# Performance work log

Hardware: AMD Instinct MI355X
Metric: run time of the kernel (lower is better)

Reference implementation:

```python
import jax, jax.numpy as jnp
import numpy as np

D_MODEL = 1024
N_HEADS = 16
D_K = 64
SEQ = 4096
BATCH = 1


def setup_inputs() -> dict:
    key = jax.random.key(0)
    ks = jax.random.split(key, 6)
    s = 1.0 / np.sqrt(D_MODEL)
    return {
        "h": jax.random.normal(ks[0], (BATCH, SEQ, D_MODEL), jnp.float32),
        "gamma": jnp.ones((D_MODEL,), jnp.float32),
        "beta": jnp.zeros((D_MODEL,), jnp.float32),
        "Wq": jax.random.normal(ks[1], (D_MODEL, N_HEADS * D_K), jnp.float32) * s,
        "bq": jnp.zeros((N_HEADS * D_K,), jnp.float32),
        "Wk": jax.random.normal(ks[2], (D_MODEL, N_HEADS * D_K), jnp.float32) * s,
        "bk": jnp.zeros((N_HEADS * D_K,), jnp.float32),
        "Wv": jax.random.normal(ks[3], (D_MODEL, N_HEADS * D_K), jnp.float32) * s,
        "bv": jnp.zeros((N_HEADS * D_K,), jnp.float32),
        "Wo": jax.random.normal(ks[4], (N_HEADS * D_K, D_MODEL), jnp.float32) * s,
        "bo": jnp.zeros((D_MODEL,), jnp.float32),
    }


def _rope(x):
    # x: [b, s, h, d]
    d = x.shape[-1]
    d2 = d // 2
    theta = 1.0 / (10000.0 ** (jnp.arange(0, d, 2, dtype=jnp.float32) / d))  # [d2]
    pos = jnp.arange(x.shape[1], dtype=jnp.float32)  # [s]
    idx_theta = pos[:, None] * theta[None, :]  # [s, d2]
    idx_theta2 = jnp.concatenate([idx_theta, idx_theta], axis=-1)  # [s, d]
    cos = jnp.cos(idx_theta2)[None, :, None, :]
    sin = jnp.sin(idx_theta2)[None, :, None, :]
    neg_half = jnp.concatenate([-x[..., d2:], x[..., :d2]], axis=-1)
    return x * cos + neg_half * sin


def reference(h, gamma, beta, Wq, bq, Wk, bk, Wv, bv, Wo, bo):
    b, s, dm = h.shape
    h_res = h
    # LayerNorm (eps=1e-5, matching torch default)
    mu = jnp.mean(h, axis=-1, keepdims=True)
    var = jnp.var(h, axis=-1, keepdims=True)
    hn = (h - mu) * jax.lax.rsqrt(var + 1e-5) * gamma + beta
    mh = (b, s, N_HEADS, D_K)
    q = (hn @ Wq + bq).reshape(mh)
    k = (hn @ Wk + bk).reshape(mh)
    v = (hn @ Wv + bv).reshape(mh)
    q = _rope(q)
    k = _rope(k)
    scale = 1.0 / np.sqrt(D_K)
    attn = jnp.einsum('bihd,bjhd->bhij', q, k) * scale  # [b,h,s,s]
    # causal mask
    mask = jnp.tril(jnp.ones((s, s), dtype=bool))
    attn = jnp.where(mask, attn, -jnp.inf)
    attn = jax.nn.softmax(attn, axis=-1)
    out = jnp.einsum('bhij,bjhd->bihd', attn, v).reshape(b, s, N_HEADS * D_K)
    return out @ Wo + bo + h_res
```

## Files before the change

### kernel.cpp

```cpp
#include <hip/hip_runtime.h>
#include <stdint.h>

#define SEQLEN 4096
#define DMODEL 1024
#define NHEADS 16
#define DKDIM  64

typedef unsigned short u16;
typedef unsigned int   u32;
using f32x4 = __attribute__((ext_vector_type(4))) float;
using i32x4 = __attribute__((ext_vector_type(4))) int;
using i32x2 = __attribute__((ext_vector_type(2))) int;
using u16x8 = __attribute__((ext_vector_type(8))) unsigned short;

__device__ __forceinline__ u16 f2bf(float f) {
    u32 x = __builtin_bit_cast(u32, f);
    u32 r = x + 0x7fffu + ((x >> 16) & 1u);
    return (u16)(r >> 16);
}
__device__ __forceinline__ float exp2a(float x) {
    float r; asm("v_exp_f32 %0, %1" : "=v"(r) : "v"(x)); return r;
}
__device__ __forceinline__ u32 cvtpk(float lo, float hi) {
    u32 r; asm("v_cvt_pk_bf16_f32 %0, %1, %2" : "=v"(r) : "v"(lo), "v"(hi)); return r;
}

__device__ __forceinline__ void mfma_bf16(f32x4& d, i32x4 a, i32x4 b) {
    asm("v_mfma_f32_16x16x32_bf16 %0, %1, %2, %0" : "+v"(d) : "v"(a), "v"(b));
}
__device__ __forceinline__ void mfma16_bf16(f32x4& d, i32x2 a, i32x2 b) {
    asm("v_mfma_f32_16x16x16_bf16 %0, %1, %2, %0" : "+v"(d) : "v"(a), "v"(b));
}

#define ASYNC_COPY16(gsrc, ldst) \
    __builtin_amdgcn_global_load_lds((const __attribute__((address_space(1))) void*)(gsrc), \
                                     (__attribute__((address_space(3))) void*)(ldst), 16, 0, 0)

__global__ __launch_bounds__(256) void prep_kernel(const float* __restrict__ Wq,
                                                   const float* __restrict__ Wk,
                                                   const float* __restrict__ Wv,
                                                   const float* __restrict__ Wo,
                                                   u16* __restrict__ wqkvT,
                                                   u16* __restrict__ woT,
                                                   const float* __restrict__ h,
                                                   const float* __restrict__ gamma,
                                                   const float* __restrict__ beta,
                                                   u16* __restrict__ hn,
                                                   float* __restrict__ cosT,
                                                   float* __restrict__ sinT) {
    __shared__ float tile[32][33];
    __shared__ float red[8];
    int bid = blockIdx.x;
    int t = threadIdx.x;
    if (bid < 4096) {
        int z = bid >> 10;
        int rem = bid & 1023;
        const float* W = (z == 0) ? Wq : (z == 1) ? Wk : (z == 2) ? Wv : Wo;
        u16* Wt = (z < 3) ? wqkvT + (size_t)z * DMODEL * DMODEL : woT;
        int bx = (rem & 31) * 32;
        int by = (rem >> 5) * 32;
        int tx = t & 31, ty = t >> 5;
#pragma unroll
        for (int i = 0; i < 32; i += 8)
            tile[ty + i][tx] = W[(size_t)(by + ty + i) * DMODEL + bx + tx];
        __syncthreads();
#pragma unroll
        for (int i = 0; i < 32; i += 8)
            Wt[(size_t)(bx + ty + i) * DMODEL + by + tx] = f2bf(tile[tx][ty + i]);
    } else if (bid < 8192) {
        int row = bid - 4096;
        float4 v = reinterpret_cast<const float4*>(h + (size_t)row * DMODEL)[t];
        float s  = v.x + v.y + v.z + v.w;
        float s2 = v.x*v.x + v.y*v.y + v.z*v.z + v.w*v.w;
#pragma unroll
        for (int off = 1; off < 64; off <<= 1) {
            s  += __shfl_xor(s, off);
            s2 += __shfl_xor(s2, off);
        }
        int wid = t >> 6, lane = t & 63;
        if (lane == 0) { red[wid] = s; red[4 + wid] = s2; }
        __syncthreads();
        s  = red[0] + red[1] + red[2] + red[3];
        s2 = red[4] + red[5] + red[6] + red[7];
        float mu   = s * (1.0f / DMODEL);
        float rstd = rsqrtf(s2 * (1.0f / DMODEL) - mu * mu + 1e-5f);
        float4 g = reinterpret_cast<const float4*>(gamma)[t];
        float4 b = reinterpret_cast<const float4*>(beta)[t];
        ushort4 o;
        o.x = f2bf((v.x - mu) * rstd * g.x + b.x);
        o.y = f2bf((v.y - mu) * rstd * g.y + b.y);
        o.z = f2bf((v.z - mu) * rstd * g.z + b.z);
        o.w = f2bf((v.w - mu) * rstd * g.w + b.w);
        reinterpret_cast<ushort4*>(hn + (size_t)row * DMODEL)[t] = o;
    } else {
        int idx = (bid - 8192) * 256 + t;
        int s = idx >> 5, i = idx & 31;
        float theta = powf(10000.0f, -2.0f * (float)i / 64.0f);
        float ang = (float)s * theta;
        cosT[idx] = cosf(ang);
        sinT[idx] = sinf(ang);
    }
}

template <int EPI>
__global__ __launch_bounds__(256) void gemm_kernel(const u16* __restrict__ A,
                                                   const u16* __restrict__ Bt,
                                                   const float* __restrict__ b0,
                                                   const float* __restrict__ b1,
                                                   const float* __restrict__ b2,
                                                   const float* __restrict__ resid,
                                                   const float* __restrict__ cosT,
                                                   const float* __restrict__ sinT,
                                                   u16* __restrict__ o0,
                                                   u16* __restrict__ o1,
                                                   u16* __restrict__ o2,
                                                   float* __restrict__ ofp) {
    __shared__ alignas(16) u16 As[2][128 * 64];
    __shared__ alignas(16) u16 Bs[2][128 * 64];
    int bm = blockIdx.x, bn = blockIdx.y;
    int tid = threadIdx.x;
    int wid = tid >> 6, lane = tid & 63;
    int wm = wid >> 1, wn = wid & 1;
    int t15 = lane & 15, g = lane >> 4;
    const u16* Abase = A  + (size_t)bm * 128 * DMODEL;
    const u16* Bbase = Bt + (size_t)bn * 128 * DMODEL;
    int srow = tid >> 3;
    int sslot = tid & 7;
    f32x4 acc[4][4] = {};

#define GSTAGE(b, ks)                                                                    \
    {                                                                                    \
        _Pragma("unroll")                                                                \
        for (int i = 0; i < 4; i++) {                                                    \
            int row = i * 32 + srow;                                                     \
            int col = ((sslot ^ (row & 7)) * 8) + (ks);                                  \
            ASYNC_COPY16(Abase + (size_t)row * DMODEL + col, &As[b][i * 2048 + wid * 512]); \
            ASYNC_COPY16(Bbase + (size_t)row * DMODEL + col, &Bs[b][i * 2048 + wid * 512]); \
        }                                                                                \
    }

    GSTAGE(0, 0)
    __syncthreads();
    int buf = 0;
    for (int ks = 0; ks < DMODEL; ks += 64) {
        if (ks < DMODEL - 64) GSTAGE(buf ^ 1, ks + 64)
#pragma unroll
        for (int kk = 0; kk < 2; kk++) {
            i32x4 af[4], bfr[4];
#pragma unroll
            for (int mi = 0; mi < 4; mi++) {
                int row = wm * 64 + mi * 16 + t15;
                int sl = (kk * 4 + g) ^ (row & 7);
                af[mi] = *reinterpret_cast<const i32x4*>(&As[buf][row * 64 + sl * 8]);
            }
#pragma unroll
            for (int ni = 0; ni < 4; ni++) {
                int row = wn * 64 + ni * 16 + t15;
                int sl = (kk * 4 + g) ^ (row & 7);
                bfr[ni] = *reinterpret_cast<const i32x4*>(&Bs[buf][row * 64 + sl * 8]);
            }
            __builtin_amdgcn_s_setprio(1);
#pragma unroll
            for (int mi = 0; mi < 4; mi++)
#pragma unroll
                for (int ni = 0; ni < 4; ni++)
                    mfma_bf16(acc[mi][ni], af[mi], bfr[ni]);
            __builtin_amdgcn_s_setprio(0);
        }
        __syncthreads();
        buf ^= 1;
    }
#undef GSTAGE

    if (EPI == 0) {
        int seg = bn >> 3;
        int bnl = bn & 7;
        const float* bias = (seg == 0) ? b0 : (seg == 1) ? b1 : b2;
        if (seg < 2) {
            u16* o = (seg == 0) ? o0 : o1;
            float qs = (seg == 0) ? 0.18033688f : 1.0f;
#pragma unroll
            for (int mi = 0; mi < 4; mi++) {
#pragma unroll
                for (int nl = 0; nl < 2; nl++) {
                    int n10 = bnl * 128 + wn * 64 + nl * 16 + t15;
                    int head = n10 >> 6;
                    int dA = n10 & 63, dB = dA + 32;
                    float bvA = bias[n10], bvB = bias[n10 + 32];
#pragma unroll
                    for (int r = 0; r < 4; r++) {
                        int m = bm * 128 + wm * 64 + mi * 16 + g * 4 + r;
                        float c  = cosT[m * 32 + dA];
                        float sn = sinT[m * 32 + dA];
                        float xA = acc[mi][nl][r] + bvA;
                        float xB = acc[mi][nl + 2][r] + bvB;
                        o[(size_t)(head * SEQLEN + m) * DKDIM + dA] = f2bf((xA * c - xB * sn) * qs);
                        o[(size_t)(head * SEQLEN + m) * DKDIM + dB] = f2bf((xB * c + xA * sn) * qs);
                    }
                }
            }
        } else {
#pragma unroll
            for (int mi = 0; mi < 4; mi++) {
#pragma unroll
                for (int ni = 0; ni < 4; ni++) {
                    int n10 = bnl * 128 + wn * 64 + ni * 16 + t15;
                    int head = n10 >> 6, dv = n10 & 63;
                    float bv = bias[n10];
                    int m = bm * 128 + wm * 64 + mi * 16 + g * 4;
                    ushort4 w4;
                    w4.x = f2bf(acc[mi][ni][0] + bv);
                    w4.y = f2bf(acc[mi][ni][1] + bv);
                    w4.z = f2bf(acc[mi][ni][2] + bv);
                    w4.w = f2bf(acc[mi][ni][3] + bv);
                    *reinterpret_cast<ushort4*>(&o2[(size_t)(head * DKDIM + dv) * SEQLEN + m]) = w4;
                }
            }
        }
    } else {
#pragma unroll
        for (int mi = 0; mi < 4; mi++) {
#pragma unroll
            for (int ni = 0; ni < 4; ni++) {
                int n = bn * 128 + wn * 64 + ni * 16 + t15;
                float bv = b0[n];
#pragma unroll
                for (int r = 0; r < 4; r++) {
                    int m = bm * 128 + wm * 64 + mi * 16 + g * 4 + r;
                    ofp[(size_t)m * DMODEL + n] = acc[mi][ni][r] + bv + resid[(size_t)m * DMODEL + n];
                }
            }
        }
    }
}

__global__ __launch_bounds__(512, 2) void attn_kernel(const u16* __restrict__ q,
                                                      const u16* __restrict__ k,
                                                      const u16* __restrict__ vt,
                                                      u16* __restrict__ o) {
    __shared__ alignas(16) u16 SMEM[65536];
    int bid = blockIdx.x;
    int h = bid & 15;
    int p = bid >> 4;
    int tid = threadIdx.x;
    int grp = tid >> 8;
    int wid = (tid >> 6) & 3;
    int lane = tid & 63;
    int t15 = lane & 15, g = lane >> 4;
    const u16* Qh  = q  + (size_t)h * SEQLEN * DKDIM;
    const u16* Kh  = k  + (size_t)h * SEQLEN * DKDIM;
    const u16* VtH = vt + (size_t)h * DKDIM * SEQLEN;
    int sslotK = lane & 7;
    int sslotV = lane & 15;
    float* Os  = (float*)SMEM;
    float2* Ml = (float2*)((char*)SMEM + 69632);

    int c7 = t15 & 7;
    int kc0e = t15 * 64 + ((g ^ c7) << 3);
    int kc1e = t15 * 64 + (((4 + g) ^ c7) << 3);
    int vce[8];
#pragma unroll
    for (int kb = 0; kb < 8; kb++)
        vce[kb] = t15 * 128 + ((((kb * 2) + (g >> 1)) ^ c7) << 3) + ((g & 1) << 2);

#define STAGE(bb, t_)                                                                   \
    {                                                                                   \
        int k0s = (t_) * 128;                                                           \
        u16* Kb = SMEM + (size_t)(grp * 2 + (bb)) * 8192;                               \
        u16* Vb = SMEM + 32768 + (size_t)(grp * 2 + (bb)) * 8192;                       \
        _Pragma("unroll")                                                               \
        for (int it = 0; it < 4; it++) {                                                \
            int u    = wid * 4 + it;                                                    \
            int krow = u * 8 + (lane >> 3);                                             \
            int ksl  = (sslotK ^ (krow & 7)) * 8;                                       \
            ASYNC_COPY16(Kh + (size_t)(k0s + krow) * DKDIM + ksl, Kb + u * 512);        \
            int vrow = u * 4 + (lane >> 4);                                             \
            int vsl  = (sslotV ^ (vrow & 7)) * 8;                                       \
            ASYNC_COPY16(VtH + (size_t)vrow * SEQLEN + k0s + vsl, Vb + u * 512);        \
        }                                                                               \
    }

    for (int pass = 0; pass < 2; pass++) {
        int Q = pass ? p : (31 - p);
        int n = Q + 1;
        int iters = (n + 1) >> 1;
        int q0 = Q * 128;
        int qrowA = q0 + wid * 32 + t15;
        int qrowB = qrowA + 16;
        i32x4 qfA0, qfA1, qfB0, qfB1;
        {
            const u16* qp = Qh + (size_t)qrowA * DKDIM + g * 8;
            qfA0 = *reinterpret_cast<const i32x4*>(qp);
            qfA1 = *reinterpret_cast<const i32x4*>(qp + 32);
            const u16* qp2 = qp + 16 * DKDIM;
            qfB0 = *reinterpret_cast<const i32x4*>(qp2);
            qfB1 = *reinterpret_cast<const i32x4*>(qp2 + 32);
        }
        f32x4 oA[4] = {}, oB[4] = {};
        float mA = -1e30f, mB = -1e30f, lA = 0.f, lB = 0.f;

        if (grp < n) STAGE(0, grp)
        __syncthreads();
        for (int i = 0; i < iters; i++) {
            int t = grp + 2 * i;
            bool active = t < n;
            int buf = i & 1;
            if (t + 2 < n) STAGE(buf ^ 1, t + 2)
            if (active) {
                int kbe = (grp * 2 + buf) * 8192;
                const u16* Kp0 = SMEM + kbe + kc0e;
                const u16* Kp1 = SMEM + kbe + kc1e;
                const u16* Vp  = SMEM + 32768 + kbe;
                int k0 = t * 128;
                f32x4 sA[8] = {}, sB[8] = {};
                __builtin_amdgcn_s_setprio(1);
#pragma unroll
                for (int kb = 0; kb < 8; kb++) {
                    i32x4 kf0 = *reinterpret_cast<const i32x4*>(Kp0 + kb * 1024);
                    i32x4 kf1 = *reinterpret_cast<const i32x4*>(Kp1 + kb * 1024);
                    mfma_bf16(sA[kb], kf0, qfA0);
                    mfma_bf16(sA[kb], kf1, qfA1);
                    mfma_bf16(sB[kb], kf0, qfB0);
                    mfma_bf16(sB[kb], kf1, qfB1);
                }
                __builtin_amdgcn_s_setprio(0);
                if (t == n - 1) {
#pragma unroll
                    for (int kb = 0; kb < 8; kb++)
#pragma unroll
                        for (int r = 0; r < 4; r++) {
                            int kvg = k0 + kb * 16 + g * 4 + r;
                            if (kvg > qrowA) sA[kb][r] = -1e30f;
                            if (kvg > qrowB) sB[kb][r] = -1e30f;
                        }
                }
                float amx[8], bmx[8];
#pragma unroll
                for (int kb = 0; kb < 8; kb++) {
                    amx[kb] = fmaxf(fmaxf(sA[kb][0], sA[kb][1]), fmaxf(sA[kb][2], sA[kb][3]));
                    bmx[kb] = fmaxf(fmaxf(sB[kb][0], sB[kb][1]), fmaxf(sB[kb][2], sB[kb][3]));
                }
                float mxA = fmaxf(fmaxf(fmaxf(amx[0], amx[1]), fmaxf(amx[2], amx[3])),
                                  fmaxf(fmaxf(amx[4], amx[5]), fmaxf(amx[6], amx[7])));
                float mxB = fmaxf(fmaxf(fmaxf(bmx[0], bmx[1]), fmaxf(bmx[2], bmx[3])),
                                  fmaxf(fmaxf(bmx[4], bmx[5]), fmaxf(bmx[6], bmx[7])));
                if (!__all((mxA <= mA + 8.0f) && (mxB <= mB + 8.0f))) {
                    float mrA = fmaxf(mxA, __shfl_xor(mxA, 16));
                    mrA = fmaxf(mrA, __shfl_xor(mrA, 32));
                    float mnA = fmaxf(mA, mrA);
                    float fdA = exp2a(mA - mnA);
                    mA = mnA; lA *= fdA;
                    oA[0] *= fdA; oA[1] *= fdA; oA[2] *= fdA; oA[3] *= fdA;
                    float mrB = fmaxf(mxB, __shfl_xor(mxB, 16));
                    mrB = fmaxf(mrB, __shfl_xor(mrB, 32));
                    float mnB = fmaxf(mB, mrB);
                    float fdB = exp2a(mB - mnB);
                    mB = mnB; lB *= fdB;
                    oB[0] *= fdB; oB[1] *= fdB; oB[2] *= fdB; oB[3] *= fdB;
                }
                float psA = 0.f, psB = 0.f;
#pragma unroll
                for (int kb = 0; kb < 8; kb++) {
                    float pa0 = exp2a(sA[kb][0] - mA);
                    float pa1 = exp2a(sA[kb][1] - mA);
                    float pa2 = exp2a(sA[kb][2] - mA);
                    float pa3 = exp2a(sA[kb][3] - mA);
                    psA += (pa0 + pa1) + (pa2 + pa3);
                    i32x2 pfA = i32x2{(int)cvtpk(pa0, pa1), (int)cvtpk(pa2, pa3)};
                    float pb0 = exp2a(sB[kb][0] - mB);
                    float pb1 = exp2a(sB[kb][1] - mB);
                    float pb2 = exp2a(sB[kb][2] - mB);
                    float pb3 = exp2a(sB[kb][3] - mB);
                    psB += (pb0 + pb1) + (pb2 + pb3);
                    i32x2 pfB = i32x2{(int)cvtpk(pb0, pb1), (int)cvtpk(pb2, pb3)};
                    __builtin_amdgcn_s_setprio(1);
#pragma unroll
                    for (int nb = 0; nb < 4; nb++) {
                        i32x2 vf = *reinterpret_cast<const i32x2*>(Vp + vce[kb] + nb * 2048);
                        mfma16_bf16(oA[nb], vf, pfA);
                        mfma16_bf16(oB[nb], vf, pfB);
                    }
                    __builtin_amdgcn_s_setprio(0);
                }
                lA += psA;
                lB += psB;
            }
            __syncthreads();
        }
        lA += __shfl_xor(lA, 16); lA += __shfl_xor(lA, 32);
        lB += __shfl_xor(lB, 16); lB += __shfl_xor(lB, 32);
        int rowA = wid * 32 + t15, rowB = rowA + 16;
#pragma unroll
        for (int nb = 0; nb < 4; nb++) {
            *reinterpret_cast<f32x4*>(&Os[(size_t)(grp * 128 + rowA) * 68 + nb * 16 + g * 4]) = oA[nb];
            *reinterpret_cast<f32x4*>(&Os[(size_t)(grp * 128 + rowB) * 68 + nb * 16 + g * 4]) = oB[nb];
        }
        if (g == 0) {
            Ml[grp * 128 + rowA] = make_float2(mA, lA);
            Ml[grp * 128 + rowB] = make_float2(mB, lB);
        }
        __syncthreads();
        {
            int r = tid >> 2, c4 = tid & 3;
            int d0 = c4 * 16;
            float2 c0 = Ml[r], c1 = Ml[128 + r];
            float M = fmaxf(c0.x, c1.x);
            float w0 = exp2a(c0.x - M), w1 = exp2a(c1.x - M);
            float invL = 1.0f / (w0 * c0.y + w1 * c1.y);
            u16* op = o + (size_t)(q0 + r) * DMODEL + h * DKDIM + d0;
#pragma unroll
            for (int j = 0; j < 2; j++) {
                f32x4 a0 = *reinterpret_cast<const f32x4*>(&Os[(size_t)r * 68 + d0 + j * 8]);
                f32x4 a1 = *reinterpret_cast<const f32x4*>(&Os[(size_t)r * 68 + d0 + j * 8 + 4]);
                f32x4 b0 = *reinterpret_cast<const f32x4*>(&Os[(size_t)(128 + r) * 68 + d0 + j * 8]);
                f32x4 b1 = *reinterpret_cast<const f32x4*>(&Os[(size_t)(128 + r) * 68 + d0 + j * 8 + 4]);
                u16x8 w8;
#pragma unroll
                for (int ii = 0; ii < 4; ii++) {
                    w8[ii]     = f2bf((w0 * a0[ii] + w1 * b0[ii]) * invL);
                    w8[4 + ii] = f2bf((w0 * a1[ii] + w1 * b1[ii]) * invL);
                }
                *reinterpret_cast<u16x8*>(op + j * 8) = w8;
            }
        }
        __syncthreads();
    }
#undef STAGE
}

extern "C" void kernel_launch(void* const* d_in, const int* in_sizes, int n_in,
                              void* d_out, int out_size, void* d_ws, size_t ws_size,
                              hipStream_t stream) {
    const float* h     = (const float*)d_in[0];
    const float* gamma = (const float*)d_in[1];
    const float* beta  = (const float*)d_in[2];
    const float* Wq    = (const float*)d_in[3];
    const float* bq    = (const float*)d_in[4];
    const float* Wk    = (const float*)d_in[5];
    const float* bk    = (const float*)d_in[6];
    const float* Wv    = (const float*)d_in[7];
    const float* bv    = (const float*)d_in[8];
    const float* Wo    = (const float*)d_in[9];
    const float* bo    = (const float*)d_in[10];
    float* out = (float*)d_out;

    char* ws = (char*)d_ws;
    u16* hn     = (u16*)(ws);
    u16* wqkvT  = (u16*)(ws + (8ull  << 20));
    u16* woT    = (u16*)(ws + (14ull << 20));
    u16* qb     = (u16*)(ws + (16ull << 20));
    u16* kbuf   = (u16*)(ws + (24ull << 20));
    u16* vtb    = (u16*)(ws + (32ull << 20));
    float* cosT = (float*)(ws + (40ull << 20));
    float* sinT = (float*)(ws + (40ull << 20) + (512ull << 10));
    u16* attn = hn;

    prep_kernel<<<8704, 256, 0, stream>>>(Wq, Wk, Wv, Wo, wqkvT, woT,
                                          h, gamma, beta, hn, cosT, sinT);
    gemm_kernel<0><<<dim3(32, 24), 256, 0, stream>>>(hn, wqkvT, bq, bk, bv, nullptr,
                                                     cosT, sinT, qb, kbuf, vtb, nullptr);
    attn_kernel<<<256, 512, 0, stream>>>(qb, kbuf, vtb, attn);
    gemm_kernel<1><<<dim3(32, 8), 256, 0, stream>>>(attn, woT, bo, nullptr, nullptr, h,
                                                    nullptr, nullptr, nullptr, nullptr, nullptr, out);
}
```

Baseline: 132.9 us.

## Replace split-KV paired-tile attention with one q-tile per block, no merge

The attention kernel drops its old scheme, where each 512-thread block handled two paired causal query tiles and split the KV range across two 256-thread groups, then merged partial results through shared memory. Now each 256-thread block handles a single 128-row query tile and walks the KV tiles sequentially with double buffering, writing normalized output directly. This removes the shared-memory merge, its extra barriers, and the pass loop, and roughly halves LDS use per block. In exchange the work per block becomes unbalanced across the causal triangle, and the grid grows to 512 blocks, so the longest blocks now run up to 32 KV tiles serially.

Result: slower. 159.8 us (+20.2%).

```diff
diff --git a/kernel.cpp b/kernel.cpp
--- a/kernel.cpp
+++ b/kernel.cpp
@@ -234,17 +234,17 @@
     }
 }
 
-__global__ __launch_bounds__(512, 2) void attn_kernel(const u16* __restrict__ q,
+__global__ __launch_bounds__(256, 2) void attn_kernel(const u16* __restrict__ q,
                                                       const u16* __restrict__ k,
                                                       const u16* __restrict__ vt,
                                                       u16* __restrict__ o) {
-    __shared__ alignas(16) u16 SMEM[65536];
+    __shared__ alignas(16) u16 Kl[2][128 * 64];
+    __shared__ alignas(16) u16 Vl[2][64 * 128];
     int bid = blockIdx.x;
     int h = bid & 15;
-    int p = bid >> 4;
+    int Q = 31 - (bid >> 4);
     int tid = threadIdx.x;
-    int grp = tid >> 8;
-    int wid = (tid >> 6) & 3;
+    int wid = tid >> 6;
     int lane = tid & 63;
     int t15 = lane & 15, g = lane >> 4;
     const u16* Qh  = q  + (size_t)h * SEQLEN * DKDIM;
@@ -252,8 +252,6 @@
     const u16* VtH = vt + (size_t)h * DKDIM * SEQLEN;
     int sslotK = lane & 7;
     int sslotV = lane & 15;
-    float* Os  = (float*)SMEM;
-    float2* Ml = (float2*)((char*)SMEM + 69632);
 
     int c7 = t15 & 7;
     int kc0e = t15 * 64 + ((g ^ c7) << 3);
@@ -266,164 +264,135 @@
 #define STAGE(bb, t_)                                                                   \
     {                                                                                   \
         int k0s = (t_) * 128;                                                           \
-        u16* Kb = SMEM + (size_t)(grp * 2 + (bb)) * 8192;                               \
-        u16* Vb = SMEM + 32768 + (size_t)(grp * 2 + (bb)) * 8192;                       \
         _Pragma("unroll")                                                               \
         for (int it = 0; it < 4; it++) {                                                \
             int u    = wid * 4 + it;                                                    \
             int krow = u * 8 + (lane >> 3);                                             \
             int ksl  = (sslotK ^ (krow & 7)) * 8;                                       \
-            ASYNC_COPY16(Kh + (size_t)(k0s + krow) * DKDIM + ksl, Kb + u * 512);        \
+            ASYNC_COPY16(Kh + (size_t)(k0s + krow) * DKDIM + ksl, &Kl[bb][u * 512]);    \
             int vrow = u * 4 + (lane >> 4);                                             \
             int vsl  = (sslotV ^ (vrow & 7)) * 8;                                       \
-            ASYNC_COPY16(VtH + (size_t)vrow * SEQLEN + k0s + vsl, Vb + u * 512);        \
+            ASYNC_COPY16(VtH + (size_t)vrow * SEQLEN + k0s + vsl, &Vl[bb][u * 512]);    \
         }                                                                               \
     }
 
-    for (int pass = 0; pass < 2; pass++) {
-        int Q = pass ? p : (31 - p);
-        int n = Q + 1;
-        int iters = (n + 1) >> 1;
-        int q0 = Q * 128;
-        int qrowA = q0 + wid * 32 + t15;
-        int qrowB = qrowA + 16;
-        i32x4 qfA0, qfA1, qfB0, qfB1;
-        {
-            const u16* qp = Qh + (size_t)qrowA * DKDIM + g * 8;
-            qfA0 = *reinterpret_cast<const i32x4*>(qp);
-            qfA1 = *reinterpret_cast<const i32x4*>(qp + 32);
-            const u16* qp2 = qp + 16 * DKDIM;
-            qfB0 = *reinterpret_cast<const i32x4*>(qp2);
-            qfB1 = *reinterpret_cast<const i32x4*>(qp2 + 32);
-        }
-        f32x4 oA[4] = {}, oB[4] = {};
-        float mA = -1e30f, mB = -1e30f, lA = 0.f, lB = 0.f;
-
-        if (grp < n) STAGE(0, grp)
+    int n = Q + 1;
+    int q0 = Q * 128;
+    int qrowA = q0 + wid * 32 + t15;
+    int qrowB = qrowA + 16;
+    i32x4 qfA0, qfA1, qfB0, qfB1;
+    {
+        const u16* qp = Qh + (size_t)qrowA * DKDIM + g * 8;
+        qfA0 = *reinterpret_cast<const i32x4*>(qp);
+        qfA1 = *reinterpret_cast<const i32x4*>(qp + 32);
+        const u16* qp2 = qp + 16 * DKDIM;
+        qfB0 = *reinterpret_cast<const i32x4*>(qp2);
+        qfB1 = *reinterpret_cast<const i32x4*>(qp2 + 32);
+    }
+    f32x4 oA[4] = {}, oB[4] = {};
+    float mA = -1e30f, mB = -1e30f, lA = 0.f, lB = 0.f;
+
+    STAGE(0, 0)
+    __syncthreads();
+    int buf = 0;
+    for (int t = 0; t < n; t++) {
+        if (t + 1 < n) STAGE(buf ^ 1, t + 1)
+        const u16* Kp0 = Kl[buf] + kc0e;
+        const u16* Kp1 = Kl[buf] + kc1e;
+        const u16* Vp  = Vl[buf];
+        int k0 = t * 128;
+        f32x4 sA[8] = {}, sB[8] = {};
+        __builtin_amdgcn_s_setprio(1);
+#pragma unroll
+        for (int kb = 0; kb < 8; kb++) {
+            i32x4 kf0 = *reinterpret_cast<const i32x4*>(Kp0 + kb * 1024);
+            i32x4 kf1 = *reinterpret_cast<const i32x4*>(Kp1 + kb * 1024);
+            mfma_bf16(sA[kb], kf0, qfA0);
+            mfma_bf16(sA[kb], kf1, qfA1);
+            mfma_bf16(sB[kb], kf0, qfB0);
+            mfma_bf16(sB[kb], kf1, qfB1);
+        }
+        __builtin_amdgcn_s_setprio(0);
+        if (t == n - 1) {
+#pragma unroll
+            for (int kb = 0; kb < 8; kb++)
+#pragma unroll
+                for (int r = 0; r < 4; r++) {
+                    int kvg = k0 + kb * 16 + g * 4 + r;
+                    if (kvg > qrowA) sA[kb][r] = -1e30f;
+                    if (kvg > qrowB) sB[kb][r] = -1e30f;
+                }
+        }
+        float amx[8], bmx[8];
+#pragma unroll
+        for (int kb = 0; kb < 8; kb++) {
+            amx[kb] = fmaxf(fmaxf(sA[kb][0], sA[kb][1]), fmaxf(sA[kb][2], sA[kb][3]));
+            bmx[kb] = fmaxf(fmaxf(sB[kb][0], sB[kb][1]), fmaxf(sB[kb][2], sB[kb][3]));
+        }
+        float mxA = fmaxf(fmaxf(fmaxf(amx[0], amx[1]), fmaxf(amx[2], amx[3])),
+                          fmaxf(fmaxf(amx[4], amx[5]), fmaxf(amx[6], amx[7])));
+        float mxB = fmaxf(fmaxf(fmaxf(bmx[0], bmx[1]), fmaxf(bmx[2], bmx[3])),
+                          fmaxf(fmaxf(bmx[4], bmx[5]), fmaxf(bmx[6], bmx[7])));
+        if (!__all((mxA <= mA + 8.0f) && (mxB <= mB + 8.0f))) {
+            float mrA = fmaxf(mxA, __shfl_xor(mxA, 16));
+            mrA = fmaxf(mrA, __shfl_xor(mrA, 32));
+            float mnA = fmaxf(mA, mrA);
+            float fdA = exp2a(mA - mnA);
+            mA = mnA; lA *= fdA;
+            oA[0] *= fdA; oA[1] *= fdA; oA[2] *= fdA; oA[3] *= fdA;
+            float mrB = fmaxf(mxB, __shfl_xor(mxB, 16));
+            mrB = fmaxf(mrB, __shfl_xor(mrB, 32));
+            float mnB = fmaxf(mB, mrB);
+            float fdB = exp2a(mB - mnB);
+            mB = mnB; lB *= fdB;
+            oB[0] *= fdB; oB[1] *= fdB; oB[2] *= fdB; oB[3] *= fdB;
+        }
+        float psA = 0.f, psB = 0.f;
+#pragma unroll
+        for (int kb = 0; kb < 8; kb++) {
+            float pa0 = exp2a(sA[kb][0] - mA);
+            float pa1 = exp2a(sA[kb][1] - mA);
+            float pa2 = exp2a(sA[kb][2] - mA);
+            float pa3 = exp2a(sA[kb][3] - mA);
+            psA += (pa0 + pa1) + (pa2 + pa3);
+            i32x2 pfA = i32x2{(int)cvtpk(pa0, pa1), (int)cvtpk(pa2, pa3)};
+            float pb0 = exp2a(sB[kb][0] - mB);
+            float pb1 = exp2a(sB[kb][1] - mB);
+            float pb2 = exp2a(sB[kb][2] - mB);
+            float pb3 = exp2a(sB[kb][3] - mB);
+            psB += (pb0 + pb1) + (pb2 + pb3);
+            i32x2 pfB = i32x2{(int)cvtpk(pb0, pb1), (int)cvtpk(pb2, pb3)};
+            __builtin_amdgcn_s_setprio(1);
+#pragma unroll
+            for (int nb = 0; nb < 4; nb++) {
+                i32x2 vf = *reinterpret_cast<const i32x2*>(Vp + vce[kb] + nb * 2048);
+                mfma16_bf16(oA[nb], vf, pfA);
+                mfma16_bf16(oB[nb], vf, pfB);
+            }
+            __builtin_amdgcn_s_setprio(0);
+        }
+        lA += psA;
+        lB += psB;
         __syncthreads();
-        for (int i = 0; i < iters; i++) {
-            int t = grp + 2 * i;
-            bool active = t < n;
-            int buf = i & 1;
-            if (t + 2 < n) STAGE(buf ^ 1, t + 2)
-            if (active) {
-                int kbe = (grp * 2 + buf) * 8192;
-                const u16* Kp0 = SMEM + kbe + kc0e;
-                const u16* Kp1 = SMEM + kbe + kc1e;
-                const u16* Vp  = SMEM + 32768 + kbe;
-                int k0 = t * 128;
-                f32x4 sA[8] = {}, sB[8] = {};
-                __builtin_amdgcn_s_setprio(1);
-#pragma unroll
-                for (int kb = 0; kb < 8; kb++) {
-                    i32x4 kf0 = *reinterpret_cast<const i32x4*>(Kp0 + kb * 1024);
-                    i32x4 kf1 = *reinterpret_cast<const i32x4*>(Kp1 + kb * 1024);
-                    mfma_bf16(sA[kb], kf0, qfA0);
-                    mfma_bf16(sA[kb], kf1, qfA1);
-                    mfma_bf16(sB[kb], kf0, qfB0);
-                    mfma_bf16(sB[kb], kf1, qfB1);
-                }
-                __builtin_amdgcn_s_setprio(0);
-                if (t == n - 1) {
-#pragma unroll
-                    for (int kb = 0; kb < 8; kb++)
-#pragma unroll
-                        for (int r = 0; r < 4; r++) {
-                            int kvg = k0 + kb * 16 + g * 4 + r;
-                            if (kvg > qrowA) sA[kb][r] = -1e30f;
-                            if (kvg > qrowB) sB[kb][r] = -1e30f;
-                        }
-                }
-                float amx[8], bmx[8];
-#pragma unroll
-                for (int kb = 0; kb < 8; kb++) {
-                    amx[kb] = fmaxf(fmaxf(sA[kb][0], sA[kb][1]), fmaxf(sA[kb][2], sA[kb][3]));
-                    bmx[kb] = fmaxf(fmaxf(sB[kb][0], sB[kb][1]), fmaxf(sB[kb][2], sB[kb][3]));
-                }
-                float mxA = fmaxf(fmaxf(fmaxf(amx[0], amx[1]), fmaxf(amx[2], amx[3])),
-                                  fmaxf(fmaxf(amx[4], amx[5]), fmaxf(amx[6], amx[7])));
-                float mxB = fmaxf(fmaxf(fmaxf(bmx[0], bmx[1]), fmaxf(bmx[2], bmx[3])),
-                                  fmaxf(fmaxf(bmx[4], bmx[5]), fmaxf(bmx[6], bmx[7])));
-                if (!__all((mxA <= mA + 8.0f) && (mxB <= mB + 8.0f))) {
-                    float mrA = fmaxf(mxA, __shfl_xor(mxA, 16));
-                    mrA = fmaxf(mrA, __shfl_xor(mrA, 32));
-                    float mnA = fmaxf(mA, mrA);
-                    float fdA = exp2a(mA - mnA);
-                    mA = mnA; lA *= fdA;
-                    oA[0] *= fdA; oA[1] *= fdA; oA[2] *= fdA; oA[3] *= fdA;
-                    float mrB = fmaxf(mxB, __shfl_xor(mxB, 16));
-                    mrB = fmaxf(mrB, __shfl_xor(mrB, 32));
-                    float mnB = fmaxf(mB, mrB);
-                    float fdB = exp2a(mB - mnB);
-                    mB = mnB; lB *= fdB;
-                    oB[0] *= fdB; oB[1] *= fdB; oB[2] *= fdB; oB[3] *= fdB;
-                }
-                float psA = 0.f, psB = 0.f;
-#pragma unroll
-                for (int kb = 0; kb < 8; kb++) {
-                    float pa0 = exp2a(sA[kb][0] - mA);
-                    float pa1 = exp2a(sA[kb][1] - mA);
-                    float pa2 = exp2a(sA[kb][2] - mA);
-                    float pa3 = exp2a(sA[kb][3] - mA);
-                    psA += (pa0 + pa1) + (pa2 + pa3);
-                    i32x2 pfA = i32x2{(int)cvtpk(pa0, pa1), (int)cvtpk(pa2, pa3)};
-                    float pb0 = exp2a(sB[kb][0] - mB);
-                    float pb1 = exp2a(sB[kb][1] - mB);
-                    float pb2 = exp2a(sB[kb][2] - mB);
-                    float pb3 = exp2a(sB[kb][3] - mB);
-                    psB += (pb0 + pb1) + (pb2 + pb3);
-                    i32x2 pfB = i32x2{(int)cvtpk(pb0, pb1), (int)cvtpk(pb2, pb3)};
-                    __builtin_amdgcn_s_setprio(1);
-#pragma unroll
-                    for (int nb = 0; nb < 4; nb++) {
-                        i32x2 vf = *reinterpret_cast<const i32x2*>(Vp + vce[kb] + nb * 2048);
-                        mfma16_bf16(oA[nb], vf, pfA);
-                        mfma16_bf16(oB[nb], vf, pfB);
-                    }
-                    __builtin_amdgcn_s_setprio(0);
-                }
-                lA += psA;
-                lB += psB;
-            }
-            __syncthreads();
-        }
-        lA += __shfl_xor(lA, 16); lA += __shfl_xor(lA, 32);
-        lB += __shfl_xor(lB, 16); lB += __shfl_xor(lB, 32);
-        int rowA = wid * 32 + t15, rowB = rowA + 16;
-#pragma unroll
-        for (int nb = 0; nb < 4; nb++) {
-            *reinterpret_cast<f32x4*>(&Os[(size_t)(grp * 128 + rowA) * 68 + nb * 16 + g * 4]) = oA[nb];
-            *reinterpret_cast<f32x4*>(&Os[(size_t)(grp * 128 + rowB) * 68 + nb * 16 + g * 4]) = oB[nb];
-        }
-        if (g == 0) {
-            Ml[grp * 128 + rowA] = make_float2(mA, lA);
-            Ml[grp * 128 + rowB] = make_float2(mB, lB);
-        }
-        __syncthreads();
-        {
-            int r = tid >> 2, c4 = tid & 3;
-            int d0 = c4 * 16;
-            float2 c0 = Ml[r], c1 = Ml[128 + r];
-            float M = fmaxf(c0.x, c1.x);
-            float w0 = exp2a(c0.x - M), w1 = exp2a(c1.x - M);
-            float invL = 1.0f / (w0 * c0.y + w1 * c1.y);
-            u16* op = o + (size_t)(q0 + r) * DMODEL + h * DKDIM + d0;
-#pragma unroll
-            for (int j = 0; j < 2; j++) {
-                f32x4 a0 = *reinterpret_cast<const f32x4*>(&Os[(size_t)r * 68 + d0 + j * 8]);
-                f32x4 a1 = *reinterpret_cast<const f32x4*>(&Os[(size_t)r * 68 + d0 + j * 8 + 4]);
-                f32x4 b0 = *reinterpret_cast<const f32x4*>(&Os[(size_t)(128 + r) * 68 + d0 + j * 8]);
-                f32x4 b1 = *reinterpret_cast<const f32x4*>(&Os[(size_t)(128 + r) * 68 + d0 + j * 8 + 4]);
-                u16x8 w8;
-#pragma unroll
-                for (int ii = 0; ii < 4; ii++) {
-                    w8[ii]     = f2bf((w0 * a0[ii] + w1 * b0[ii]) * invL);
-                    w8[4 + ii] = f2bf((w0 * a1[ii] + w1 * b1[ii]) * invL);
-                }
-                *reinterpret_cast<u16x8*>(op + j * 8) = w8;
-            }
-        }
-        __syncthreads();
+        buf ^= 1;
+    }
+    lA += __shfl_xor(lA, 16); lA += __shfl_xor(lA, 32);
+    lB += __shfl_xor(lB, 16); lB += __shfl_xor(lB, 32);
+    float invA = 1.0f / lA;
+    float invB = 1.0f / lB;
+#pragma unroll
+    for (int nb = 0; nb < 4; nb++) {
+        ushort4 w4;
+        w4.x = f2bf(oA[nb][0] * invA);
+        w4.y = f2bf(oA[nb][1] * invA);
+        w4.z = f2bf(oA[nb][2] * invA);
+        w4.w = f2bf(oA[nb][3] * invA);
+        *reinterpret_cast<ushort4*>(&o[(size_t)qrowA * DMODEL + h * DKDIM + nb * 16 + g * 4]) = w4;
+        w4.x = f2bf(oB[nb][0] * invB);
+        w4.y = f2bf(oB[nb][1] * invB);
+        w4.z = f2bf(oB[nb][2] * invB);
+        w4.w = f2bf(oB[nb][3] * invB);
+        *reinterpret_cast<ushort4*>(&o[(size_t)qrowB * DMODEL + h * DKDIM + nb * 16 + g * 4]) = w4;
     }
 #undef STAGE
 }
@@ -459,7 +428,7 @@
                                           h, gamma, beta, hn, cosT, sinT);
     gemm_kernel<0><<<dim3(32, 24), 256, 0, stream>>>(hn, wqkvT, bq, bk, bv, nullptr,
                                                      cosT, sinT, qb, kbuf, vtb, nullptr);
-    attn_kernel<<<256, 512, 0, stream>>>(qb, kbuf, vtb, attn);
+    attn_kernel<<<512, 256, 0, stream>>>(qb, kbuf, vtb, attn);
     gemm_kernel<1><<<dim3(32, 8), 256, 0, stream>>>(attn, woT, bo, nullptr, nullptr, h,
                                                     nullptr, nullptr, nullptr, nullptr, nullptr, out);
 }
```
